# Optimization experiments

Hardware: AMD Instinct MI355X
Metric: run time of the kernel (lower is better)

The kernel has to match this reference:

```python
import jax, jax.numpy as jnp
import numpy as np

N_HEAD = 16
LN_EPS = 1e-5


def _ln(x, w, b):
    # torch LayerNorm computed in float32 then cast back (see LayerNorm.forward)
    xf = x.astype(jnp.float32)
    mu = jnp.mean(xf, axis=-1, keepdims=True)
    var = jnp.mean(jnp.square(xf - mu), axis=-1, keepdims=True)
    return ((xf - mu) * jax.lax.rsqrt(var + LN_EPS) * w + b).astype(x.dtype)


def setup_inputs() -> dict:
    key = jax.random.key(0)
    ks = jax.random.split(key, 16)
    B, S, C = 4, 1500, 1024
    A = 256  # adapter_dim
    F = 4 * C
    s = 0.02
    return {
        "x": jax.random.normal(ks[0], (B, S, C), jnp.float32),
        "Wq": jax.random.normal(ks[1], (C, C), jnp.float32) * s,
        "bq": jnp.zeros((C,), jnp.float32),
        "Wk": jax.random.normal(ks[2], (C, C), jnp.float32) * s,
        "Wv": jax.random.normal(ks[3], (C, C), jnp.float32) * s,
        "bv": jnp.zeros((C,), jnp.float32),
        "Wo": jax.random.normal(ks[4], (C, C), jnp.float32) * s,
        "bo": jnp.zeros((C,), jnp.float32),
        "ln_attn_w": jnp.ones((C,), jnp.float32),
        "ln_attn_b": jnp.zeros((C,), jnp.float32),
        "W1": jax.random.normal(ks[5], (F, C), jnp.float32) * s,
        "b1": jnp.zeros((F,), jnp.float32),
        "W2": jax.random.normal(ks[6], (C, F), jnp.float32) * s,
        "b2": jnp.zeros((C,), jnp.float32),
        "ln_mlp_w": jnp.ones((C,), jnp.float32),
        "ln_mlp_b": jnp.zeros((C,), jnp.float32),
        "Wds": jax.random.normal(ks[7], (A, C), jnp.float32) * s,
        "bds": jnp.zeros((A,), jnp.float32),
        "Wus": jax.random.normal(ks[8], (C, A), jnp.float32) * s,
        "bus": jnp.zeros((C,), jnp.float32),
    }


def reference(x, Wq, bq, Wk, Wv, bv, Wo, bo, ln_attn_w, ln_attn_b,
              W1, b1, W2, b2, ln_mlp_w, ln_mlp_b, Wds, bds, Wus, bus):
    B, S, C = x.shape
    H = N_HEAD
    D = C // H
    scale = D ** -0.25  # applied to both q and k, per qkv_attention

    # --- self-attention ---
    h = _ln(x, ln_attn_w, ln_attn_b)
    q = (h @ Wq.T + bq).reshape(B, S, H, D) * scale
    k = (h @ Wk.T).reshape(B, S, H, D) * scale  # key has no bias
    v = (h @ Wv.T + bv).reshape(B, S, H, D)
    qk = jnp.einsum("bqhd,bkhd->bhqk", q, k).astype(jnp.float32)
    w = jax.nn.softmax(qk, axis=-1).astype(x.dtype)
    wv = jnp.einsum("bhqk,bkhd->bqhd", w, v).reshape(B, S, C)
    x = x + (wv @ Wo.T + bo)

    # --- MLP (exact GELU, as nn.GELU default) ---
    h = _ln(x, ln_mlp_w, ln_mlp_b)
    x = x + (jax.nn.gelu(h @ W1.T + b1, approximate=False) @ W2.T + b2)

    # --- bottleneck adapter: x + us(gelu(ds(x))) ---
    x = x + (jax.nn.gelu(x @ Wds.T + bds, approximate=False) @ Wus.T + bus)
    return x
```

## Files before the change

kernel.cpp:

```cpp
#include <hip/hip_runtime.h>
#include <hip/hip_bf16.h>
#include <math.h>

typedef __bf16 bf16;
typedef __bf16 bf16x8 __attribute__((ext_vector_type(8)));
typedef float  f32x4  __attribute__((ext_vector_type(4)));

__device__ __forceinline__ void load16_lds(const bf16* g, bf16* l) {
    __builtin_amdgcn_global_load_lds(
        (__attribute__((address_space(1))) void*)(g),
        (__attribute__((address_space(3))) void*)(l), 16, 0, 0);
}

__device__ __forceinline__ float gelu_f(float x) {
    float u = 1.5957691216057308f * (x + 0.044715f * x * x * x);
    float e = __expf(u);
    float th = 1.0f - 2.0f / (1.0f + e);
    return 0.5f * x * (1.0f + th);
}

struct ConvArgs {
    const float* src[19];
    bf16* dst[19];
    int n[19];
    int bstart[20];
};
__global__ __launch_bounds__(256) void convert_many(ConvArgs a) {
    int blk = blockIdx.x;
    int s = 0;
    while (blk >= a.bstart[s + 1]) s++;
    const float* src = a.src[s];
    bf16* dst = a.dst[s];
    int n = a.n[s];
    int i0 = (blk - a.bstart[s]) * 2048;
#pragma unroll
    for (int e = 0; e < 8; e++) {
        int i = i0 + threadIdx.x + e * 256;
        if (i < n) dst[i] = (bf16)src[i];
    }
}

__global__ void zero_kernel(bf16* dst, int n) {
    int i = blockIdx.x * blockDim.x + threadIdx.x;
    if (i < n) dst[i] = (bf16)0.0f;
}

template<int ACT, int RES>
__global__ __launch_bounds__(256) void reduce_kernel(
    const bf16* __restrict__ P0, const bf16* __restrict__ P1,
    const bf16* __restrict__ bias, const bf16* __restrict__ resid,
    bf16* __restrict__ out, int nmask, int total)
{
    int i = (blockIdx.x * 256 + threadIdx.x) * 8;
    if (i >= total) return;
    bf16x8 p0 = *(const bf16x8*)(P0 + i);
    bf16x8 p1 = *(const bf16x8*)(P1 + i);
    bf16x8 bb = *(const bf16x8*)(bias + (i & nmask));
    bf16x8 rr;
    if (RES) rr = *(const bf16x8*)(resid + i);
    bf16x8 o;
#pragma unroll
    for (int j = 0; j < 8; j++) {
        float v = (float)p0[j] + (float)p1[j] + (float)bb[j];
        if (ACT) v = gelu_f(v);
        if (RES) v += (float)rr[j];
        o[j] = (bf16)v;
    }
    *(bf16x8*)(out + i) = o;
}

template<class XT>
__global__ __launch_bounds__(256) void ln_kernel(
    const XT* __restrict__ X, const bf16* __restrict__ w,
    const bf16* __restrict__ b, bf16* __restrict__ out)
{
    const int C = 1024;
    const int row = blockIdx.x;
    const int tid = threadIdx.x;
    const XT* xr = X + (size_t)row * C;
    float x0 = (float)xr[tid * 4 + 0], x1 = (float)xr[tid * 4 + 1];
    float x2 = (float)xr[tid * 4 + 2], x3 = (float)xr[tid * 4 + 3];
    float s  = x0 + x1 + x2 + x3;
    float sq = x0*x0 + x1*x1 + x2*x2 + x3*x3;
#pragma unroll
    for (int off = 32; off >= 1; off >>= 1) {
        s  += __shfl_xor(s,  off, 64);
        sq += __shfl_xor(sq, off, 64);
    }
    __shared__ float red[8];
    int wave = tid >> 6;
    if ((tid & 63) == 0) { red[wave] = s; red[4 + wave] = sq; }
    __syncthreads();
    float ts = red[0] + red[1] + red[2] + red[3];
    float tq = red[4] + red[5] + red[6] + red[7];
    float mean = ts * (1.0f / C);
    float var  = tq * (1.0f / C) - mean * mean;
    float rstd = rsqrtf(var + 1e-5f);
    float w0 = (float)w[tid*4+0], w1 = (float)w[tid*4+1], w2 = (float)w[tid*4+2], w3 = (float)w[tid*4+3];
    float b0 = (float)b[tid*4+0], b1 = (float)b[tid*4+1], b2 = (float)b[tid*4+2], b3 = (float)b[tid*4+3];
    bf16* orow = out + (size_t)row * C + tid * 4;
    orow[0] = (bf16)((x0 - mean) * rstd * w0 + b0);
    orow[1] = (bf16)((x1 - mean) * rstd * w1 + b1);
    orow[2] = (bf16)((x2 - mean) * rstd * w2 + b2);
    orow[3] = (bf16)((x3 - mean) * rstd * w3 + b3);
}

template<int ACT, int OMODE, class RT, class OT>
__global__ __launch_bounds__(256) void gemm_kernel(
    const bf16* __restrict__ A, const bf16* __restrict__ W,
    const bf16* __restrict__ bias, const RT* __restrict__ resid,
    OT* __restrict__ out, bf16* __restrict__ out_k, bf16* __restrict__ out_v,
    int M, int N, int K, float scale, int gmT, int gnT, int mQ, int ldK)
{
    const int lin = blockIdx.x;
    const int xcd = lin & 7;
    const int t_  = lin >> 3;
    const int mt_ = (xcd & 3) + 4 * (t_ % mQ);
    const int nt_ = (xcd >> 2) + 2 * (t_ / mQ);
    if (mt_ >= gmT || nt_ >= gnT) return;
    const int m0 = mt_ * 128;
    const int n0 = nt_ * 128;
    const int ksp = (OMODE == 3) ? blockIdx.y : 0;
    const size_t ko = (size_t)ksp * K;

    __shared__ __align__(16) bf16 As[16 * 512];
    __shared__ __align__(16) bf16 Bs[16 * 512];
    const int tid = threadIdx.x;
    const int wave = tid >> 6, lane = tid & 63;
    const int lane15 = lane & 15, quad = lane >> 4;
    const int wm0 = (wave >> 1) * 64;
    const int wn0 = (wave & 1) * 64;
    f32x4 acc[4][4] = {};

    int ra0 = m0 + (2 * wave)     * 16 + lane15; if (ra0 > M - 1) ra0 = M - 1;
    int ra1 = m0 + (2 * wave + 1) * 16 + lane15; if (ra1 > M - 1) ra1 = M - 1;
    const int rb0 = n0 + (2 * wave)     * 16 + lane15;
    const int rb1 = n0 + (2 * wave + 1) * 16 + lane15;
    const bf16* a0 = A + (size_t)ra0 * ldK + ko + quad * 8;
    const bf16* a1 = A + (size_t)ra1 * ldK + ko + quad * 8;
    const bf16* w0 = W + (size_t)rb0 * ldK + ko + quad * 8;
    const bf16* w1 = W + (size_t)rb1 * ldK + ko + quad * 8;

    for (int k0 = 0; k0 < K; k0 += 64) {
#pragma unroll
        for (int kk = 0; kk < 2; kk++) {
            load16_lds(a0 + k0 + kk * 32, &As[((2 * wave)     * 2 + kk) * 512]);
            load16_lds(a1 + k0 + kk * 32, &As[((2 * wave + 1) * 2 + kk) * 512]);
            load16_lds(w0 + k0 + kk * 32, &Bs[((2 * wave)     * 2 + kk) * 512]);
            load16_lds(w1 + k0 + kk * 32, &Bs[((2 * wave + 1) * 2 + kk) * 512]);
        }
        __syncthreads();
#pragma unroll
        for (int kk = 0; kk < 2; kk++) {
            bf16x8 af[4], bfr[4];
#pragma unroll
            for (int tt = 0; tt < 4; tt++) {
                af[tt]  = *(const bf16x8*)(&As[(((wm0 >> 4) + tt) * 2 + kk) * 512 + lane * 8]);
                bfr[tt] = *(const bf16x8*)(&Bs[(((wn0 >> 4) + tt) * 2 + kk) * 512 + lane * 8]);
            }
#pragma unroll
            for (int mt = 0; mt < 4; mt++)
#pragma unroll
                for (int nt = 0; nt < 4; nt++)
                    acc[mt][nt] = __builtin_amdgcn_mfma_f32_16x16x32_bf16(
                        af[mt], bfr[nt], acc[mt][nt], 0, 0, 0);
        }
        __syncthreads();
    }

#pragma unroll
    for (int mt = 0; mt < 4; mt++) {
#pragma unroll
        for (int r = 0; r < 4; r++) {
            int gm = m0 + wm0 + mt * 16 + quad * 4 + r;
            if (gm >= M) continue;
#pragma unroll
            for (int nt = 0; nt < 4; nt++) {
                int gn = n0 + wn0 + nt * 16 + lane15;
                float v = acc[mt][nt][r];
                if (OMODE == 3) {
                    bf16* po = ksp ? out_k : (bf16*)out;
                    po[(size_t)gm * N + gn] = (bf16)v;
                    continue;
                }
                if (bias) v += (float)bias[gn];
                if (OMODE == 2) {
                    if (gn < 2048) {
                        v *= scale;
                        if (gn < 1024) v *= 1.4426950408889634f;
                    }
                } else v *= scale;
                if (ACT == 1) v = gelu_f(v);
                if (OMODE == 2) {
                    if (gn < 1024) {
                        ((bf16*)out)[(size_t)gm * 1024 + gn] = (bf16)v;
                    } else if (gn < 2048) {
                        out_k[(size_t)gm * 1024 + (gn - 1024)] = (bf16)v;
                    } else {
                        int gg = gn - 2048;
                        int bb = gm / 1500;
                        int ss = gm - bb * 1500;
                        int hh = gg >> 6, dd = gg & 63;
                        out_v[(((size_t)bb * 16 + hh) * 64 + dd) * 1536 + ss] = (bf16)v;
                    }
                } else {
                    if (resid) v += (float)resid[(size_t)gm * N + gn];
                    out[(size_t)gm * N + gn] = (OT)v;
                }
            }
        }
    }
}

__global__ __launch_bounds__(256) void flash_attn_kernel(
    const bf16* __restrict__ Q, const bf16* __restrict__ Km,
    const bf16* __restrict__ Vt, bf16* __restrict__ O)
{
    const int S = 1500, C = 1024, SP = 1536;
    const int LDP = 72;
    __shared__ __align__(16) bf16 Ks[2][8 * 512];
    __shared__ __align__(16) bf16 Vs[2][8 * 512];
    __shared__ __align__(16) bf16 Ps[4 * 16 * LDP];
    const int tid = threadIdx.x;
    const int wave = tid >> 6, lane = tid & 63;
    const int lane15 = lane & 15, quad = lane >> 4;
    const int bh = blockIdx.y;
    const int q0 = blockIdx.x * 64;
    const size_t headoff = (size_t)(bh >> 4) * S * C + (size_t)(bh & 15) * 64;
    const size_t vtoff   = (size_t)bh * 64 * SP;

    bf16x8 qf[2];
    int qr = q0 + wave * 16 + lane15; if (qr > S - 1) qr = S - 1;
    qf[0] = *(const bf16x8*)(Q + headoff + (size_t)qr * C + quad * 8);
    qf[1] = *(const bf16x8*)(Q + headoff + (size_t)qr * C + 32 + quad * 8);

    const bf16* vbase = Vt + vtoff + (size_t)(wave * 16 + lane15) * SP + quad * 8;

    auto stageKV = [&](int buf, int kt) {
        const int j0 = kt * 64;
        int kr = j0 + wave * 16 + lane15; if (kr > S - 1) kr = S - 1;
        const bf16* kbase = Km + headoff + (size_t)kr * C + quad * 8;
#pragma unroll
        for (int kk = 0; kk < 2; kk++) {
            load16_lds(kbase + kk * 32,      &Ks[buf][(wave * 2 + kk) * 512]);
            load16_lds(vbase + j0 + kk * 32, &Vs[buf][(wave * 2 + kk) * 512]);
        }
    };

    float m_run[4], l_part[4];
    f32x4 o_acc[4] = {};
#pragma unroll
    for (int r = 0; r < 4; r++) { m_run[r] = 4.0f; l_part[r] = 0.0f; }

    stageKV(0, 0);
    asm volatile("s_waitcnt vmcnt(0)" ::: "memory");
    __builtin_amdgcn_s_barrier();
    __builtin_amdgcn_sched_barrier(0);

    int cur = 0;
    for (int kt = 0; kt < 24; kt++) {
        if (kt + 1 < 24) stageKV(cur ^ 1, kt + 1);
        const int j0 = kt * 64;

        f32x4 s[4] = {};
#pragma unroll
        for (int kk = 0; kk < 2; kk++) {
#pragma unroll
            for (int nt = 0; nt < 4; nt++) {
                bf16x8 kf = *(const bf16x8*)(&Ks[cur][(nt * 2 + kk) * 512 + lane * 8]);
                s[nt] = __builtin_amdgcn_mfma_f32_16x16x32_bf16(qf[kk], kf, s[nt], 0, 0, 0);
            }
        }
        if (kt == 23) {
#pragma unroll
            for (int nt = 0; nt < 4; nt++) {
                if (j0 + nt * 16 + lane15 >= S) {
#pragma unroll
                    for (int r = 0; r < 4; r++) s[nt][r] = -1e30f;
                }
            }
        }

        float tm[4];
#pragma unroll
        for (int r = 0; r < 4; r++)
            tm[r] = fmaxf(fmaxf(s[0][r], s[1][r]), fmaxf(s[2][r], s[3][r]));
        bool rec = (tm[0] > m_run[0]) | (tm[1] > m_run[1]) |
                   (tm[2] > m_run[2]) | (tm[3] > m_run[3]);
        if (__any(rec)) {
#pragma unroll
            for (int r = 0; r < 4; r++) {
                float rm = tm[r];
#pragma unroll
                for (int off = 1; off < 16; off <<= 1) rm = fmaxf(rm, __shfl_xor(rm, off, 64));
                float mnew  = fmaxf(m_run[r], rm);
                float alpha = __builtin_amdgcn_exp2f(m_run[r] - mnew);
                m_run[r] = mnew;
                l_part[r] *= alpha;
#pragma unroll
                for (int dt = 0; dt < 4; dt++) o_acc[dt][r] *= alpha;
            }
        }

#pragma unroll
        for (int nt = 0; nt < 4; nt++) {
#pragma unroll
            for (int r = 0; r < 4; r++) {
                float p = __builtin_amdgcn_exp2f(s[nt][r] - m_run[r]);
                l_part[r] += p;
                Ps[wave * 16 * LDP + (quad * 4 + r) * LDP + nt * 16 + lane15] = (bf16)p;
            }
        }
        asm volatile("s_waitcnt lgkmcnt(0)" ::: "memory");
        __builtin_amdgcn_sched_barrier(0);
#pragma unroll
        for (int kk = 0; kk < 2; kk++) {
            bf16x8 pf = *(const bf16x8*)(&Ps[wave * 16 * LDP + lane15 * LDP + kk * 32 + quad * 8]);
#pragma unroll
            for (int dt = 0; dt < 4; dt++) {
                bf16x8 vf = *(const bf16x8*)(&Vs[cur][(dt * 2 + kk) * 512 + lane * 8]);
                o_acc[dt] = __builtin_amdgcn_mfma_f32_16x16x32_bf16(pf, vf, o_acc[dt], 0, 0, 0);
            }
        }
        if (kt + 1 < 24) {
            asm volatile("s_waitcnt vmcnt(0)" ::: "memory");
            __builtin_amdgcn_s_barrier();
            __builtin_amdgcn_sched_barrier(0);
        }
        cur ^= 1;
    }

    float l_inv[4];
#pragma unroll
    for (int r = 0; r < 4; r++) {
        float ls = l_part[r];
#pragma unroll
        for (int off = 1; off < 16; off <<= 1) ls += __shfl_xor(ls, off, 64);
        l_inv[r] = 1.0f / ls;
    }

#pragma unroll
    for (int dt = 0; dt < 4; dt++) {
#pragma unroll
        for (int r = 0; r < 4; r++) {
            int row = q0 + wave * 16 + quad * 4 + r;
            if (row < S) {
                float v = o_acc[dt][r] * l_inv[r];
                O[headoff + (size_t)row * C + dt * 16 + lane15] = (bf16)v;
            }
        }
    }
}

extern "C" void kernel_launch(void* const* d_in, const int* in_sizes, int n_in,
                              void* d_out, int out_size, void* d_ws, size_t ws_size,
                              hipStream_t stream) {
    float* out = (float*)d_out;
    const float* x_f32 = (const float*)d_in[0];
    const int M = 6000, Cc = 1024, F = 4096, Aa = 256;
    const size_t MC = (size_t)M * Cc;
    const size_t VT_ELEMS = (size_t)64 * 64 * 1536;
    bf16* ws = (bf16*)d_ws;

    bf16* h1   = ws;
    bf16* kbuf = ws + MC;
    bf16* Vt   = ws + 2 * MC;
    bf16* g    = ws + 2 * MC + VT_ELEMS;
    bf16* q    = (bf16*)d_out;
    bf16* wv   = h1;
    bf16* x1   = q;
    bf16* h2   = kbuf;
    bf16* x2   = Vt;
    bf16* aact = kbuf;
    bf16* P0   = kbuf;
    bf16* P1   = h1;
    bf16* P0d  = h1;
    bf16* P1d  = h1 + (size_t)M * Aa;

    size_t off = 2 * MC + VT_ELEMS + (size_t)M * F;
    bf16* Wqkv = ws + off; off += (size_t)3 * 1024 * 1024;
    bf16* bqkv = ws + off; off += 3072;
    bf16* sWo  = ws + off; off += (size_t)1024 * 1024;
    bf16* sbo  = ws + off; off += 1024;
    bf16* slnw = ws + off; off += 1024;
    bf16* slnb = ws + off; off += 1024;
    bf16* sW1  = ws + off; off += (size_t)4096 * 1024;
    bf16* sb1  = ws + off; off += 4096;
    bf16* sW2  = ws + off; off += (size_t)1024 * 4096;
    bf16* sb2  = ws + off; off += 1024;
    bf16* sln2w = ws + off; off += 1024;
    bf16* sln2b = ws + off; off += 1024;
    bf16* sWds = ws + off; off += (size_t)256 * 1024;
    bf16* sbds = ws + off; off += 256;
    bf16* sWus = ws + off; off += (size_t)1024 * 256;
    bf16* sbus = ws + off; off += 1024;

    ConvArgs ca;
    const int srcidx[19] = {1, 3, 4, 2, 5, 6, 7, 8, 9, 10, 11, 12, 13, 14, 15, 16, 17, 18, 19};
    bf16* dsts[19] = {Wqkv, Wqkv + 1048576, Wqkv + 2097152, bqkv, bqkv + 2048,
                      sWo, sbo, slnw, slnb, sW1, sb1, sW2, sb2, sln2w, sln2b,
                      sWds, sbds, sWus, sbus};
    int bacc = 0;
    for (int i = 0; i < 19; i++) {
        ca.src[i] = (const float*)d_in[srcidx[i]];
        ca.dst[i] = dsts[i];
        ca.n[i] = in_sizes[srcidx[i]];
        ca.bstart[i] = bacc;
        bacc += (ca.n[i] + 2047) / 2048;
    }
    ca.bstart[19] = bacc;

    dim3 blk(256);
    convert_many<<<bacc, blk, 0, stream>>>(ca);
    zero_kernel<<<4, blk, 0, stream>>>(bqkv + 1024, 1024);

    const float scale = 0.35355339059327373f;
    const int gmT = 47, mQ = 12;
    auto grid_for = [&](int gnT) { int nQ = (gnT + 1) >> 1; return dim3(8 * mQ * nQ); };

    ln_kernel<float><<<M, blk, 0, stream>>>(x_f32, slnw, slnb, h1);
    gemm_kernel<0, 2, bf16, bf16><<<grid_for(24), blk, 0, stream>>>(
        h1, Wqkv, bqkv, (const bf16*)nullptr, q, kbuf, Vt, M, 3072, Cc, scale, gmT, 24, mQ, Cc);
    dim3 ga(24, 64);
    flash_attn_kernel<<<ga, blk, 0, stream>>>(q, kbuf, Vt, wv);
    gemm_kernel<0, 0, float, bf16><<<grid_for(8), blk, 0, stream>>>(
        wv, sWo, sbo, x_f32, x1, nullptr, nullptr, M, Cc, Cc, 1.0f, gmT, 8, mQ, Cc);
    ln_kernel<bf16><<<M, blk, 0, stream>>>(x1, sln2w, sln2b, h2);
    gemm_kernel<1, 0, bf16, bf16><<<grid_for(32), blk, 0, stream>>>(
        h2, sW1, sb1, (const bf16*)nullptr, g, nullptr, nullptr, M, F, Cc, 1.0f, gmT, 32, mQ, Cc);

    {
        dim3 gr = grid_for(8); gr.y = 2;
        gemm_kernel<0, 3, bf16, bf16><<<gr, blk, 0, stream>>>(
            g, sW2, nullptr, (const bf16*)nullptr, P0, P1, nullptr,
            M, Cc, F / 2, 1.0f, gmT, 8, mQ, F);
        reduce_kernel<0, 1><<<(M * Cc) / 2048, blk, 0, stream>>>(
            P0, P1, sb2, x1, x2, Cc - 1, M * Cc);
    }

    {
        dim3 gr = grid_for(2); gr.y = 2;
        gemm_kernel<0, 3, bf16, bf16><<<gr, blk, 0, stream>>>(
            x2, sWds, nullptr, (const bf16*)nullptr, P0d, P1d, nullptr,
            M, Aa, Cc / 2, 1.0f, gmT, 2, mQ, Cc);
        reduce_kernel<1, 0><<<(M * Aa) / 2048, blk, 0, stream>>>(
            P0d, P1d, sbds, nullptr, aact, Aa - 1, M * Aa);
    }

    gemm_kernel<0, 0, bf16, float><<<grid_for(8), blk, 0, stream>>>(
        aact, sWus, sbus, x2, out, nullptr, nullptr, M, Cc, Aa, 1.0f, gmT, 8, mQ, Aa);
}
```

Baseline: 756.3 us.

## Double GEMM K-tile depth and split-K the Wo and up-projection GEMMs

Makes the GEMM K-step a template parameter and raises it from 64 to 128 for every GEMM. This halves the number of barrier-separated load/compute iterations but doubles LDS per block, which may lower occupancy. The Wo projection and the adapter up-projection now use 2-way split-K into bf16 partial buffers, followed by a reduce kernel that adds bias and residual. That gives those N=1024 GEMMs twice as many blocks, at the cost of extra partial-buffer traffic, an extra launch, and a scalar rather than vectorised reduce store path.

```diff
diff --git a/kernel.cpp b/kernel.cpp
--- a/kernel.cpp
+++ b/kernel.cpp
@@ -45,28 +45,24 @@
     if (i < n) dst[i] = (bf16)0.0f;
 }
 
-template<int ACT, int RES>
+template<int ACT, int RES, class RT, class OT>
 __global__ __launch_bounds__(256) void reduce_kernel(
     const bf16* __restrict__ P0, const bf16* __restrict__ P1,
-    const bf16* __restrict__ bias, const bf16* __restrict__ resid,
-    bf16* __restrict__ out, int nmask, int total)
+    const bf16* __restrict__ bias, const RT* __restrict__ resid,
+    OT* __restrict__ out, int nmask, int total)
 {
     int i = (blockIdx.x * 256 + threadIdx.x) * 8;
     if (i >= total) return;
     bf16x8 p0 = *(const bf16x8*)(P0 + i);
     bf16x8 p1 = *(const bf16x8*)(P1 + i);
     bf16x8 bb = *(const bf16x8*)(bias + (i & nmask));
-    bf16x8 rr;
-    if (RES) rr = *(const bf16x8*)(resid + i);
-    bf16x8 o;
 #pragma unroll
     for (int j = 0; j < 8; j++) {
         float v = (float)p0[j] + (float)p1[j] + (float)bb[j];
         if (ACT) v = gelu_f(v);
-        if (RES) v += (float)rr[j];
-        o[j] = (bf16)v;
-    }
-    *(bf16x8*)(out + i) = o;
+        if (RES) v += (float)resid[i + j];
+        out[i + j] = (OT)v;
+    }
 }
 
 template<class XT>
@@ -105,7 +101,7 @@
     orow[3] = (bf16)((x3 - mean) * rstd * w3 + b3);
 }
 
-template<int ACT, int OMODE, class RT, class OT>
+template<int ACT, int OMODE, int BK2, class RT, class OT>
 __global__ __launch_bounds__(256) void gemm_kernel(
     const bf16* __restrict__ A, const bf16* __restrict__ W,
     const bf16* __restrict__ bias, const RT* __restrict__ resid,
@@ -123,8 +119,8 @@
     const int ksp = (OMODE == 3) ? blockIdx.y : 0;
     const size_t ko = (size_t)ksp * K;
 
-    __shared__ __align__(16) bf16 As[16 * 512];
-    __shared__ __align__(16) bf16 Bs[16 * 512];
+    __shared__ __align__(16) bf16 As[8 * BK2 * 512];
+    __shared__ __align__(16) bf16 Bs[8 * BK2 * 512];
     const int tid = threadIdx.x;
     const int wave = tid >> 6, lane = tid & 63;
     const int lane15 = lane & 15, quad = lane >> 4;
@@ -141,22 +137,22 @@
     const bf16* w0 = W + (size_t)rb0 * ldK + ko + quad * 8;
     const bf16* w1 = W + (size_t)rb1 * ldK + ko + quad * 8;
 
-    for (int k0 = 0; k0 < K; k0 += 64) {
-#pragma unroll
-        for (int kk = 0; kk < 2; kk++) {
-            load16_lds(a0 + k0 + kk * 32, &As[((2 * wave)     * 2 + kk) * 512]);
-            load16_lds(a1 + k0 + kk * 32, &As[((2 * wave + 1) * 2 + kk) * 512]);
-            load16_lds(w0 + k0 + kk * 32, &Bs[((2 * wave)     * 2 + kk) * 512]);
-            load16_lds(w1 + k0 + kk * 32, &Bs[((2 * wave + 1) * 2 + kk) * 512]);
+    for (int k0 = 0; k0 < K; k0 += 32 * BK2) {
+#pragma unroll
+        for (int kk = 0; kk < BK2; kk++) {
+            load16_lds(a0 + k0 + kk * 32, &As[((2 * wave)     * BK2 + kk) * 512]);
+            load16_lds(a1 + k0 + kk * 32, &As[((2 * wave + 1) * BK2 + kk) * 512]);
+            load16_lds(w0 + k0 + kk * 32, &Bs[((2 * wave)     * BK2 + kk) * 512]);
+            load16_lds(w1 + k0 + kk * 32, &Bs[((2 * wave + 1) * BK2 + kk) * 512]);
         }
         __syncthreads();
 #pragma unroll
-        for (int kk = 0; kk < 2; kk++) {
+        for (int kk = 0; kk < BK2; kk++) {
             bf16x8 af[4], bfr[4];
 #pragma unroll
             for (int tt = 0; tt < 4; tt++) {
-                af[tt]  = *(const bf16x8*)(&As[(((wm0 >> 4) + tt) * 2 + kk) * 512 + lane * 8]);
-                bfr[tt] = *(const bf16x8*)(&Bs[(((wn0 >> 4) + tt) * 2 + kk) * 512 + lane * 8]);
+                af[tt]  = *(const bf16x8*)(&As[(((wm0 >> 4) + tt) * BK2 + kk) * 512 + lane * 8]);
+                bfr[tt] = *(const bf16x8*)(&Bs[(((wn0 >> 4) + tt) * BK2 + kk) * 512 + lane * 8]);
             }
 #pragma unroll
             for (int mt = 0; mt < 4; mt++)
@@ -372,10 +368,14 @@
     bf16* h2   = kbuf;
     bf16* x2   = Vt;
     bf16* aact = kbuf;
+    bf16* P0o  = kbuf;
+    bf16* P1o  = g;
     bf16* P0   = kbuf;
     bf16* P1   = h1;
     bf16* P0d  = h1;
     bf16* P1d  = h1 + (size_t)M * Aa;
+    bf16* P0u  = g;
+    bf16* P1u  = g + MC;
 
     size_t off = 2 * MC + VT_ELEMS + (size_t)M * F;
     bf16* Wqkv = ws + off; off += (size_t)3 * 1024 * 1024;
@@ -419,34 +419,48 @@
     auto grid_for = [&](int gnT) { int nQ = (gnT + 1) >> 1; return dim3(8 * mQ * nQ); };
 
     ln_kernel<float><<<M, blk, 0, stream>>>(x_f32, slnw, slnb, h1);
-    gemm_kernel<0, 2, bf16, bf16><<<grid_for(24), blk, 0, stream>>>(
+    gemm_kernel<0, 2, 4, bf16, bf16><<<grid_for(24), blk, 0, stream>>>(
         h1, Wqkv, bqkv, (const bf16*)nullptr, q, kbuf, Vt, M, 3072, Cc, scale, gmT, 24, mQ, Cc);
     dim3 ga(24, 64);
     flash_attn_kernel<<<ga, blk, 0, stream>>>(q, kbuf, Vt, wv);
-    gemm_kernel<0, 0, float, bf16><<<grid_for(8), blk, 0, stream>>>(
-        wv, sWo, sbo, x_f32, x1, nullptr, nullptr, M, Cc, Cc, 1.0f, gmT, 8, mQ, Cc);
-    ln_kernel<bf16><<<M, blk, 0, stream>>>(x1, sln2w, sln2b, h2);
-    gemm_kernel<1, 0, bf16, bf16><<<grid_for(32), blk, 0, stream>>>(
-        h2, sW1, sb1, (const bf16*)nullptr, g, nullptr, nullptr, M, F, Cc, 1.0f, gmT, 32, mQ, Cc);
 
     {
         dim3 gr = grid_for(8); gr.y = 2;
-        gemm_kernel<0, 3, bf16, bf16><<<gr, blk, 0, stream>>>(
+        gemm_kernel<0, 3, 4, bf16, bf16><<<gr, blk, 0, stream>>>(
+            wv, sWo, nullptr, (const bf16*)nullptr, P0o, P1o, nullptr,
+            M, Cc, Cc / 2, 1.0f, gmT, 8, mQ, Cc);
+        reduce_kernel<0, 1, float, bf16><<<(M * Cc) / 2048, blk, 0, stream>>>(
+            P0o, P1o, sbo, x_f32, x1, Cc - 1, M * Cc);
+    }
+
+    ln_kernel<bf16><<<M, blk, 0, stream>>>(x1, sln2w, sln2b, h2);
+    gemm_kernel<1, 0, 4, bf16, bf16><<<grid_for(32), blk, 0, stream>>>(
+        h2, sW1, sb1, (const bf16*)nullptr, g, nullptr, nullptr, M, F, Cc, 1.0f, gmT, 32, mQ, Cc);
+
+    {
+        dim3 gr = grid_for(8); gr.y = 2;
+        gemm_kernel<0, 3, 4, bf16, bf16><<<gr, blk, 0, stream>>>(
             g, sW2, nullptr, (const bf16*)nullptr, P0, P1, nullptr,
             M, Cc, F / 2, 1.0f, gmT, 8, mQ, F);
-        reduce_kernel<0, 1><<<(M * Cc) / 2048, blk, 0, stream>>>(
+        reduce_kernel<0, 1, bf16, bf16><<<(M * Cc) / 2048, blk, 0, stream>>>(
             P0, P1, sb2, x1, x2, Cc - 1, M * Cc);
     }
 
     {
         dim3 gr = grid_for(2); gr.y = 2;
-        gemm_kernel<0, 3, bf16, bf16><<<gr, blk, 0, stream>>>(
+        gemm_kernel<0, 3, 4, bf16, bf16><<<gr, blk, 0, stream>>>(
             x2, sWds, nullptr, (const bf16*)nullptr, P0d, P1d, nullptr,
             M, Aa, Cc / 2, 1.0f, gmT, 2, mQ, Cc);
-        reduce_kernel<1, 0><<<(M * Aa) / 2048, blk, 0, stream>>>(
+        reduce_kernel<1, 0, bf16, bf16><<<(M * Aa) / 2048, blk, 0, stream>>>(
             P0d, P1d, sbds, nullptr, aact, Aa - 1, M * Aa);
     }
 
-    gemm_kernel<0, 0, bf16, float><<<grid_for(8), blk, 0, stream>>>(
-        aact, sWus, sbus, x2, out, nullptr, nullptr, M, Cc, Aa, 1.0f, gmT, 8, mQ, Aa);
-}
+    {
+        dim3 gr = grid_for(8); gr.y = 2;
+        gemm_kernel<0, 3, 4, bf16, bf16><<<gr, blk, 0, stream>>>(
+            aact, sWus, nullptr, (const bf16*)nullptr, P0u, P1u, nullptr,
+            M, Cc, Aa / 2, 1.0f, gmT, 8, mQ, Aa);
+        reduce_kernel<0, 1, bf16, float><<<(M * Cc) / 2048, blk, 0, stream>>>(
+            P0u, P1u, sbus, x2, out, Cc - 1, M * Cc);
+    }
+}
```

After: 750.6 us. Within noise of the previous version (-0.8%).
